# Optimization experiments

Hardware: AMD Instinct MI355X
Metric: run time of the kernel (lower is better)

Reference implementation:

```python
import jax, jax.numpy as jnp
import numpy as np

EMBED_DIM = 1024
NUM_HEADS = 16
HEAD_DIM = EMBED_DIM // NUM_HEADS


def setup_inputs() -> dict:
    key = jax.random.key(0)
    ks = jax.random.split(key, 9)
    B, S, D = 2, 2048, EMBED_DIM
    scale = 1.0 / np.sqrt(D)
    x = jax.random.normal(ks[0], (B, S, D), dtype=jnp.float32)
    # Linear params (torch nn.Linear: y = x @ W.T + b); store W as [out, in]
    Wq = jax.random.normal(ks[1], (D, D), dtype=jnp.float32) * scale
    bq = jnp.zeros((D,), dtype=jnp.float32)
    Wk = jax.random.normal(ks[2], (D, D), dtype=jnp.float32) * scale
    bk = jnp.zeros((D,), dtype=jnp.float32)
    Wv = jax.random.normal(ks[3], (D, D), dtype=jnp.float32) * scale
    bv = jnp.zeros((D,), dtype=jnp.float32)
    Wo = jax.random.normal(ks[4], (D, D), dtype=jnp.float32) * scale
    bo = jnp.zeros((D,), dtype=jnp.float32)
    return {"x": x, "Wq": Wq, "bq": bq, "Wk": Wk, "bk": bk,
            "Wv": Wv, "bv": bv, "Wo": Wo, "bo": bo}


def reference(x, Wq, bq, Wk, bk, Wv, bv, Wo, bo):
    B, S, D = x.shape
    H, Hd = NUM_HEADS, HEAD_DIM
    scaling = Hd ** -0.5
    # projections (torch Linear: x @ W.T + b)
    q = (x @ Wq.T + bq).reshape(B, S, H, Hd).transpose(0, 2, 1, 3)  # [B,H,S,Hd]
    k = (x @ Wk.T + bk).reshape(B, S, H, Hd).transpose(0, 2, 1, 3)
    v = (x @ Wv.T + bv).reshape(B, S, H, Hd).transpose(0, 2, 1, 3)
    # full score matrix, as in the original (no flash tiling)
    scores = jnp.einsum('bhqd,bhkd->bhqk', q, k) * scaling  # [B,H,S,S]
    attn = jax.nn.softmax(scores, axis=-1)
    # dropout is identity in eval mode
    out = jnp.einsum('bhqk,bhkd->bhqd', attn, v)  # [B,H,S,Hd]
    out = out.transpose(0, 2, 1, 3).reshape(B, S, D)
    return out @ Wo.T + bo
```

## Files before the change

kernel.cpp:

```cpp
#include <hip/hip_runtime.h>
#include <stdint.h>

typedef unsigned short u16;
typedef short short8 __attribute__((ext_vector_type(8)));
typedef float f32x4 __attribute__((ext_vector_type(4)));
typedef float f32x16 __attribute__((ext_vector_type(16)));
typedef float f32x2 __attribute__((ext_vector_type(2)));

__device__ __forceinline__ u16 f2bf_fast(float f) {
  union { float f; uint32_t u; } x;
  x.f = f;
  return (u16)((x.u + 0x8000u) >> 16);
}

__device__ __forceinline__ uint32_t pack2bf(float lo, float hi) {
  union { float f; uint32_t u; } a, b;
  a.f = lo; b.f = hi;
  return __builtin_amdgcn_perm(b.u + 0x8000u, a.u + 0x8000u, 0x07060302u);
}

__device__ __forceinline__ float bf2f(uint32_t u) {
  union { uint32_t u; float f; } x;
  x.u = u << 16;
  return x.f;
}

__device__ __forceinline__ uint32_t cvtpk(float lo, float hi) {
  uint32_t r;
  asm("v_cvt_pk_bf16_f32 %0, %1, %2" : "=v"(r) : "v"(lo), "v"(hi));
  return r;
}

__device__ __forceinline__ void permswap(uint32_t& a, uint32_t& b) {
  asm("v_permlane32_swap_b32 %0, %1" : "+v"(a), "+v"(b));
}

__device__ __forceinline__ void gload_lds16(const void* g, void* l) {
  __builtin_amdgcn_global_load_lds(
      (const __attribute__((address_space(1))) void*)g,
      (__attribute__((address_space(3))) void*)l, 16, 0, 0);
}

__device__ __forceinline__ f32x4 mfma16(short8 a, short8 b, f32x4 c) {
  return __builtin_amdgcn_mfma_f32_16x16x32_bf16(a, b, c, 0, 0, 0);
}

__device__ __forceinline__ f32x16 mfma32(short8 a, short8 b, f32x16 c) {
  return __builtin_amdgcn_mfma_f32_32x32x16_bf16(a, b, c, 0, 0, 0);
}

__device__ __forceinline__ short8 ldfrag(const u16* base, int tile, int kc,
                                         int lane) {
  return *(const short8*)(base + ((((tile << 5) + kc) << 6) + lane) * 8);
}

#define QSCALE 0.18033688011112042f

__global__ void pack_all(const float* __restrict__ x, const float* __restrict__ wq,
                         const float* __restrict__ wk, const float* __restrict__ wv,
                         const float* __restrict__ wo, u16* __restrict__ xp,
                         u16* __restrict__ wp) {
  const int gi = blockIdx.x * 256 + threadIdx.x;
  const int lane = gi & 63;
  const int kc = (gi >> 6) & 31;
  const int rt = gi >> 11;
  const int col = kc * 32 + (lane >> 4) * 8;
  const float* src;
  int row;
  if (rt < 256) {
    src = x;
    row = rt * 16 + (lane & 15);
  } else {
    const int wti = rt - 256;
    const int widx = wti >> 6;
    src = (widx == 0) ? wq : (widx == 1) ? wk : (widx == 2) ? wv : wo;
    row = (wti & 63) * 16 + (lane & 15);
  }
  const float4* p = (const float4*)(src + (size_t)row * 1024 + col);
  const float4 v0 = p[0], v1 = p[1];
  uint4 o;
  o.x = pack2bf(v0.x, v0.y);
  o.y = pack2bf(v0.z, v0.w);
  o.z = pack2bf(v1.x, v1.y);
  o.w = pack2bf(v1.z, v1.w);
  u16* dst = (rt < 256) ? xp : wp;
  const int og = (rt < 256) ? gi : gi - 524288;
  ((uint4*)dst)[og] = o;
}

__global__ __launch_bounds__(256, 3) void proj_qkv(
    const u16* __restrict__ xp, const u16* __restrict__ wp,
    const float* __restrict__ bq, const float* __restrict__ bk,
    const float* __restrict__ bv, u16* __restrict__ qw, u16* __restrict__ kw,
    u16* __restrict__ vw) {
  const int gid = blockIdx.x * 4 + (threadIdx.x >> 6);
  const int lane = threadIdx.x & 63;
  const int quad = lane >> 4, l15 = lane & 15;
  const bool isQK = gid < 2048;
  int at0, bt0, bm, bn;
  const u16 *Ap, *Bp;
  if (isQK) {
    bn = gid >> 6; bm = gid & 63;
    Ap = xp; at0 = bm * 4;
    Bp = wp; bt0 = bn * 4;
  } else {
    const int h = gid - 2048;
    bn = h & 63; bm = h >> 6;
    Ap = wp; at0 = 128 + bm * 4;
    Bp = xp; bt0 = bn * 4;
  }

  f32x4 acc[4][4] = {};
  short8 af[2][4], bf[2][4];
#pragma unroll
  for (int mt = 0; mt < 4; ++mt) af[0][mt] = ldfrag(Ap, at0 + mt, 0, lane);
#pragma unroll
  for (int nt = 0; nt < 4; ++nt) bf[0][nt] = ldfrag(Bp, bt0 + nt, 0, lane);

#pragma unroll 4
  for (int kc = 0; kc < 32; ++kc) {
    const int cur = kc & 1, nxt = cur ^ 1;
    if (kc < 31) {
#pragma unroll
      for (int mt = 0; mt < 4; ++mt)
        af[nxt][mt] = ldfrag(Ap, at0 + mt, kc + 1, lane);
#pragma unroll
      for (int nt = 0; nt < 4; ++nt)
        bf[nxt][nt] = ldfrag(Bp, bt0 + nt, kc + 1, lane);
    }
#pragma unroll
    for (int mt = 0; mt < 4; ++mt)
#pragma unroll
      for (int nt = 0; nt < 4; ++nt)
        acc[mt][nt] = mfma16(af[cur][mt], bf[cur][nt], acc[mt][nt]);
  }

#pragma unroll
  for (int nt = 0; nt < 4; ++nt) {
    const int n = bn * 64 + nt * 16 + l15;
#pragma unroll
    for (int mt = 0; mt < 4; ++mt)
#pragma unroll
      for (int r = 0; r < 4; ++r) {
        const int m = bm * 64 + mt * 16 + quad * 4 + r;
        const float a = acc[mt][nt][r];
        if (isQK) {
          const bool isQ = (bn < 16);
          const int nn = isQ ? n : n - 1024;
          const float v = isQ ? (a + bq[nn]) * QSCALE : a + bk[nn];
          u16* op = isQ ? qw : kw;
          const int b = m >> 11, s = m & 2047, hh = nn >> 6, d = nn & 63;
          op[((size_t)((b * 16 + hh) * 2048 + s)) * 64 + d] = f2bf_fast(v);
        } else {
          const float v = a + bv[m];
          const int b = n >> 11, s = n & 2047;
          vw[((size_t)(b * 1024 + m)) * 2048 + s] = f2bf_fast(v);
        }
      }
  }
}

__global__ __launch_bounds__(256, 4) void attn_kernel(
    const u16* __restrict__ Q, const u16* __restrict__ Kt,
    const u16* __restrict__ Vt, u16* __restrict__ op0, u16* __restrict__ op1,
    float* __restrict__ lp) {
  __shared__ __align__(16) u16 Sm[16384];
  const int tid = threadIdx.x, lane = tid & 63, w = tid >> 6;
  const int l31 = lane & 31, hi = lane >> 5, l7 = lane & 7;
  const int qt = blockIdx.x;
  const int bh = blockIdx.y >> 1;
  const int ks = blockIdx.y & 1;

  const char* Qb = (const char*)(Q + ((size_t)bh * 2048 + qt * 128) * 64);
  const char* Kb = (const char*)(Kt + ((size_t)bh * 2048 + ks * 1024) * 64);
  const char* Vb = (const char*)(Vt + (size_t)bh * 64 * 2048 + ks * 1024);

  auto stageKV = [&](int kt, int b) {
    u16* Kl = Sm + b * 4096;
    u16* Vl = Sm + 8192 + b * 4096;
#pragma unroll
    for (int i = 0; i < 2; ++i) {
      const int G = (w * 2 + i) * 64 + lane;
      const int r = G >> 3, sl = G & 7;
      gload_lds16(Kb + (size_t)(kt * 64 + r) * 128 + ((sl ^ (r & 7)) * 16),
                  &Kl[G * 8]);
      gload_lds16(Vb + (size_t)r * 4096 + kt * 128 + ((sl ^ (r & 7)) * 16),
                  &Vl[G * 8]);
    }
  };

#pragma unroll
  for (int i = 0; i < 4; ++i) {
    const int G = (w * 4 + i) * 64 + lane;
    const int row = G >> 3, sl = G & 7;
    u16* qdst = (G < 512) ? (Sm + 4096) : (Sm + 12288);
    gload_lds16(Qb + (size_t)row * 128 + ((sl ^ (row & 7)) * 16),
                &qdst[(G & 511) * 8]);
  }
  stageKV(0, 0);
  __syncthreads();

  const u16* qreg = (w < 2) ? (Sm + 4096) : (Sm + 12288);
  const int qr0 = (w & 1) * 32;
  short8 aq[4];
#pragma unroll
  for (int ds = 0; ds < 4; ++ds)
    aq[ds] = *(const short8*)&qreg[(qr0 + l31) * 64 + (((ds << 1) + hi) ^ l7) * 8];
  __syncthreads();

  f32x16 ot[2] = {};
  f32x2 l2 = {0.f, 0.f};

  for (int kt = 0; kt < 16; ++kt) {
    const int buf = kt & 1;
    if (kt < 15) stageKV(kt + 1, buf ^ 1);
    const u16* Kl = Sm + buf * 4096;
    const u16* Vl = Sm + 8192 + buf * 4096;

#pragma unroll
    for (int t = 0; t < 2; ++t) {
      f32x16 st = {};
#pragma unroll
      for (int ds = 0; ds < 4; ++ds) {
        short8 kf = *(const short8*)&Kl[(t * 32 + l31) * 64 +
                                        (((ds << 1) + hi) ^ l7) * 8];
        st = mfma32(kf, aq[ds], st);
      }
      float e[16];
#pragma unroll
      for (int i = 0; i < 16; ++i) e[i] = __builtin_amdgcn_exp2f(st[i]);
#pragma unroll
      for (int i = 0; i < 8; ++i) l2 += (f32x2){e[2 * i], e[2 * i + 1]};

      uint32_t p01 = cvtpk(e[0], e[1]),   p23 = cvtpk(e[2], e[3]);
      uint32_t p45 = cvtpk(e[4], e[5]),   p67 = cvtpk(e[6], e[7]);
      uint32_t p89 = cvtpk(e[8], e[9]),   pAB = cvtpk(e[10], e[11]);
      uint32_t pCD = cvtpk(e[12], e[13]), pEF = cvtpk(e[14], e[15]);
      permswap(p01, p45);
      permswap(p23, p67);
      permswap(p89, pCD);
      permswap(pAB, pEF);
      union { uint32_t u[4]; short8 s; } b0, b1;
      b0.u[0] = p01; b0.u[1] = p23; b0.u[2] = p45; b0.u[3] = p67;
      b1.u[0] = p89; b1.u[1] = pAB; b1.u[2] = pCD; b1.u[3] = pEF;

#pragma unroll
      for (int dt = 0; dt < 2; ++dt) {
#pragma unroll
        for (int s2 = 0; s2 < 2; ++s2) {
          short8 vf = *(const short8*)&Vl[(dt * 32 + l31) * 64 +
                                          ((((t * 2 + s2) << 1) + hi) ^ l7) * 8];
          ot[dt] = mfma32(vf, s2 ? b1.s : b0.s, ot[dt]);
        }
      }
    }
    if (kt < 15) __syncthreads();
  }

  const int b = bh >> 4, h = bh & 15;
  u16* op = ks ? op1 : op0;
  float l = l2.x + l2.y;
  l += __shfl_xor(l, 32);
  const int srow = qt * 128 + w * 32 + l31;
  if (hi == 0) lp[((size_t)(ks * 32 + bh)) * 2048 + srow] = l;
  const int rt = b * 128 + qt * 8 + w * 2 + (l31 >> 4);
#pragma unroll
  for (int dt = 0; dt < 2; ++dt) {
    const int kc = h * 2 + dt;
#pragma unroll
    for (int g = 0; g < 4; ++g) {
      const int ln = (lane & 15) + 16 * g;
      uint2 ov;
      ov.x = cvtpk(ot[dt][4 * g + 0], ot[dt][4 * g + 1]);
      ov.y = cvtpk(ot[dt][4 * g + 2], ot[dt][4 * g + 3]);
      *(uint2*)(op + ((size_t)((rt * 32 + kc) * 64 + ln)) * 8 + hi * 4) = ov;
    }
  }
}

__global__ void attn_combine(const u16* __restrict__ op0,
                             const u16* __restrict__ op1,
                             const float* __restrict__ lp,
                             u16* __restrict__ awp) {
  const int g = blockIdx.x * 256 + threadIdx.x;
  const int ln = g & 63;
  const int kc = (g >> 6) & 31;
  const int rt = g >> 11;
  const int row = rt * 16 + (ln & 15);
  const int b = row >> 11, s = row & 2047;
  const int h = kc >> 1;
  const int lidx = (b * 16 + h) * 2048 + s;
  const float inv = __builtin_amdgcn_rcpf(lp[lidx] + lp[lidx + 65536]);
  const uint4 a0 = ((const uint4*)op0)[g];
  const uint4 a1 = ((const uint4*)op1)[g];
  uint4 o;
  o.x = pack2bf((bf2f(a0.x) + bf2f(a1.x)) * inv,
                (bf2f(a0.x >> 16) + bf2f(a1.x >> 16)) * inv);
  o.y = pack2bf((bf2f(a0.y) + bf2f(a1.y)) * inv,
                (bf2f(a0.y >> 16) + bf2f(a1.y >> 16)) * inv);
  o.z = pack2bf((bf2f(a0.z) + bf2f(a1.z)) * inv,
                (bf2f(a0.z >> 16) + bf2f(a1.z >> 16)) * inv);
  o.w = pack2bf((bf2f(a0.w) + bf2f(a1.w)) * inv,
                (bf2f(a0.w >> 16) + bf2f(a1.w >> 16)) * inv);
  ((uint4*)awp)[g] = o;
}

__global__ __launch_bounds__(256, 3) void out_proj(const u16* __restrict__ awp,
                                                   const u16* __restrict__ wp,
                                                   const float* __restrict__ bo,
                                                   float* __restrict__ out) {
  const int gid = blockIdx.x * 4 + (threadIdx.x >> 6);
  const int lane = threadIdx.x & 63;
  const int quad = lane >> 4, l15 = lane & 15;
  const int bm = gid & 63, bnn = gid >> 6;
  const int at0 = bm * 4, bt0 = 192 + bnn * 2;

  f32x4 acc[4][2] = {};
  short8 af[2][4], bf[2][2];
#pragma unroll
  for (int mt = 0; mt < 4; ++mt) af[0][mt] = ldfrag(awp, at0 + mt, 0, lane);
#pragma unroll
  for (int nt = 0; nt < 2; ++nt) bf[0][nt] = ldfrag(wp, bt0 + nt, 0, lane);

#pragma unroll 4
  for (int kc = 0; kc < 32; ++kc) {
    const int cur = kc & 1, nxt = cur ^ 1;
    if (kc < 31) {
#pragma unroll
      for (int mt = 0; mt < 4; ++mt)
        af[nxt][mt] = ldfrag(awp, at0 + mt, kc + 1, lane);
#pragma unroll
      for (int nt = 0; nt < 2; ++nt)
        bf[nxt][nt] = ldfrag(wp, bt0 + nt, kc + 1, lane);
    }
#pragma unroll
    for (int mt = 0; mt < 4; ++mt)
#pragma unroll
      for (int nt = 0; nt < 2; ++nt)
        acc[mt][nt] = mfma16(af[cur][mt], bf[cur][nt], acc[mt][nt]);
  }

#pragma unroll
  for (int nt = 0; nt < 2; ++nt) {
    const int n = bnn * 32 + nt * 16 + l15;
    const float bb = bo[n];
#pragma unroll
    for (int mt = 0; mt < 4; ++mt)
#pragma unroll
      for (int r = 0; r < 4; ++r) {
        const int m = bm * 64 + mt * 16 + quad * 4 + r;
        out[(size_t)m * 1024 + n] = acc[mt][nt][r] + bb;
      }
  }
}

extern "C" void kernel_launch(void* const* d_in, const int* in_sizes, int n_in,
                              void* d_out, int out_size, void* d_ws, size_t ws_size,
                              hipStream_t stream) {
  const float* x  = (const float*)d_in[0];
  const float* Wq = (const float*)d_in[1];
  const float* bq = (const float*)d_in[2];
  const float* Wk = (const float*)d_in[3];
  const float* bk = (const float*)d_in[4];
  const float* Wv = (const float*)d_in[5];
  const float* bv = (const float*)d_in[6];
  const float* Wo = (const float*)d_in[7];
  const float* bo = (const float*)d_in[8];

  const size_t M4 = (size_t)4 * 1024 * 1024;
  u16* xp  = (u16*)d_ws;
  u16* wp  = xp + M4;
  u16* qw  = wp + M4;
  u16* kw  = qw + M4;
  u16* vw  = kw + M4;
  u16* op1 = vw + M4;
  u16* awp = op1 + M4;
  float* lp = (float*)(awp + M4);
  u16* op0 = xp;

  pack_all<<<4096, 256, 0, stream>>>(x, Wq, Wk, Wv, Wo, xp, wp);

  proj_qkv<<<768, 256, 0, stream>>>(xp, wp, bq, bk, bv, qw, kw, vw);

  attn_kernel<<<dim3(16, 64), 256, 0, stream>>>(qw, kw, vw, op0, op1, lp);

  attn_combine<<<2048, 256, 0, stream>>>(op0, op1, lp, awp);

  out_proj<<<512, 256, 0, stream>>>(awp, wp, bo, (float*)d_out);
}
```

Baseline: 199.1 us.

## Stage projection GEMM tiles through LDS shared across waves with XCD-aware block mapping

The QKV and output projection GEMMs move from per-wave direct global fragment loads to block-level 128x128 tiles staged in LDS via global_load_lds. Each wave then reads its fragments from shared memory, so A and B tiles are reused across waves and global traffic drops. Block indices are remapped so neighbouring tiles land on the same XCD for better L2 reuse. The staging is single-buffered with two barriers per k-step, which removes the previous register double-buffering and may expose load latency.

```diff
diff --git a/kernel.cpp b/kernel.cpp
--- a/kernel.cpp
+++ b/kernel.cpp
@@ -47,11 +47,6 @@
 
 __device__ __forceinline__ f32x16 mfma32(short8 a, short8 b, f32x16 c) {
   return __builtin_amdgcn_mfma_f32_32x32x16_bf16(a, b, c, 0, 0, 0);
-}
-
-__device__ __forceinline__ short8 ldfrag(const u16* base, int tile, int kc,
-                                         int lane) {
-  return *(const short8*)(base + ((((tile << 5) + kc) << 6) + lane) * 8);
 }
 
 #define QSCALE 0.18033688011112042f
@@ -93,46 +88,65 @@
     const float* __restrict__ bq, const float* __restrict__ bk,
     const float* __restrict__ bv, u16* __restrict__ qw, u16* __restrict__ kw,
     u16* __restrict__ vw) {
-  const int gid = blockIdx.x * 4 + (threadIdx.x >> 6);
-  const int lane = threadIdx.x & 63;
+  __shared__ __align__(16) u16 As[8192];
+  __shared__ __align__(16) u16 Bs[8192];
+  const int tid = threadIdx.x, lane = tid & 63, w = tid >> 6;
   const int quad = lane >> 4, l15 = lane & 15;
-  const bool isQK = gid < 2048;
-  int at0, bt0, bm, bn;
+
+  const int bid = blockIdx.x;
+  const int work = (bid & 7) * 96 + (bid >> 3);
+  const bool isQK = work < 512;
+  int at0, bt0, bm2, bn2;
   const u16 *Ap, *Bp;
   if (isQK) {
-    bn = gid >> 6; bm = gid & 63;
-    Ap = xp; at0 = bm * 4;
-    Bp = wp; bt0 = bn * 4;
+    bm2 = work >> 4; bn2 = work & 15;
+    Ap = xp; at0 = bm2 * 8;
+    Bp = wp; bt0 = bn2 * 8;
   } else {
-    const int h = gid - 2048;
-    bn = h & 63; bm = h >> 6;
-    Ap = wp; at0 = 128 + bm * 4;
-    Bp = xp; bt0 = bn * 4;
-  }
+    const int h = work - 512;
+    bm2 = h >> 5; bn2 = h & 31;
+    Ap = wp; at0 = 128 + bm2 * 8;
+    Bp = xp; bt0 = bn2 * 8;
+  }
+  const int wr = w >> 1, wc = w & 1;
+  const int bm = bm2 * 2 + wr, bn = bn2 * 2 + wc;
 
   f32x4 acc[4][4] = {};
-  short8 af[2][4], bf[2][4];
-#pragma unroll
-  for (int mt = 0; mt < 4; ++mt) af[0][mt] = ldfrag(Ap, at0 + mt, 0, lane);
-#pragma unroll
-  for (int nt = 0; nt < 4; ++nt) bf[0][nt] = ldfrag(Bp, bt0 + nt, 0, lane);
-
-#pragma unroll 4
-  for (int kc = 0; kc < 32; ++kc) {
-    const int cur = kc & 1, nxt = cur ^ 1;
-    if (kc < 31) {
+
+  for (int ks = 0; ks < 16; ++ks) {
+    const int kc0 = ks * 2;
+#pragma unroll
+    for (int i = 0; i < 8; ++i) {
+      const int g = w * 8 + i;
+      const int gg = g & 15, t = gg >> 1, c = gg & 1;
+      const u16* src = (g < 16)
+          ? (Ap + ((((at0 + t) << 5) + kc0 + c) * 64 + lane) * 8)
+          : (Bp + ((((bt0 + t) << 5) + kc0 + c) * 64 + lane) * 8);
+      u16* dst = ((g < 16) ? As : Bs) + (gg * 64 + lane) * 8;
+      gload_lds16(src, dst);
+    }
+    __syncthreads();
+
+    short8 af[4][2], bf[4][2];
+#pragma unroll
+    for (int mt = 0; mt < 4; ++mt)
+#pragma unroll
+      for (int c = 0; c < 2; ++c)
+        af[mt][c] = *(const short8*)&As[((((wr * 4 + mt) << 1) + c) * 64 + lane) * 8];
+#pragma unroll
+    for (int nt = 0; nt < 4; ++nt)
+#pragma unroll
+      for (int c = 0; c < 2; ++c)
+        bf[nt][c] = *(const short8*)&Bs[((((wc * 4 + nt) << 1) + c) * 64 + lane) * 8];
+
+#pragma unroll
+    for (int c = 0; c < 2; ++c)
 #pragma unroll
       for (int mt = 0; mt < 4; ++mt)
-        af[nxt][mt] = ldfrag(Ap, at0 + mt, kc + 1, lane);
-#pragma unroll
-      for (int nt = 0; nt < 4; ++nt)
-        bf[nxt][nt] = ldfrag(Bp, bt0 + nt, kc + 1, lane);
-    }
-#pragma unroll
-    for (int mt = 0; mt < 4; ++mt)
-#pragma unroll
-      for (int nt = 0; nt < 4; ++nt)
-        acc[mt][nt] = mfma16(af[cur][mt], bf[cur][nt], acc[mt][nt]);
+#pragma unroll
+        for (int nt = 0; nt < 4; ++nt)
+          acc[mt][nt] = mfma16(af[mt][c], bf[nt][c], acc[mt][nt]);
+    __syncthreads();
   }
 
 #pragma unroll
@@ -305,50 +319,68 @@
   ((uint4*)awp)[g] = o;
 }
 
-__global__ __launch_bounds__(256, 3) void out_proj(const u16* __restrict__ awp,
+__global__ __launch_bounds__(512, 2) void out_proj(const u16* __restrict__ awp,
                                                    const u16* __restrict__ wp,
                                                    const float* __restrict__ bo,
                                                    float* __restrict__ out) {
-  const int gid = blockIdx.x * 4 + (threadIdx.x >> 6);
-  const int lane = threadIdx.x & 63;
+  __shared__ __align__(16) u16 As[8192];
+  __shared__ __align__(16) u16 Bs[8192];
+  const int tid = threadIdx.x, lane = tid & 63, w = tid >> 6;
   const int quad = lane >> 4, l15 = lane & 15;
-  const int bm = gid & 63, bnn = gid >> 6;
-  const int at0 = bm * 4, bt0 = 192 + bnn * 2;
+
+  const int bid = blockIdx.x;
+  const int work = (bid & 7) * 32 + (bid >> 3);
+  const int bm2 = work >> 3, bn2 = work & 7;
+  const int at0 = bm2 * 8, bt0 = 192 + bn2 * 8;
+  const int wr = w >> 2, wc = w & 3;
 
   f32x4 acc[4][2] = {};
-  short8 af[2][4], bf[2][2];
-#pragma unroll
-  for (int mt = 0; mt < 4; ++mt) af[0][mt] = ldfrag(awp, at0 + mt, 0, lane);
-#pragma unroll
-  for (int nt = 0; nt < 2; ++nt) bf[0][nt] = ldfrag(wp, bt0 + nt, 0, lane);
-
-#pragma unroll 4
-  for (int kc = 0; kc < 32; ++kc) {
-    const int cur = kc & 1, nxt = cur ^ 1;
-    if (kc < 31) {
+
+  for (int ks = 0; ks < 16; ++ks) {
+    const int kc0 = ks * 2;
+#pragma unroll
+    for (int i = 0; i < 4; ++i) {
+      const int g = w * 4 + i;
+      const int gg = g & 15, t = gg >> 1, c = gg & 1;
+      const u16* src = (g < 16)
+          ? (awp + ((((at0 + t) << 5) + kc0 + c) * 64 + lane) * 8)
+          : (wp + ((((bt0 + t) << 5) + kc0 + c) * 64 + lane) * 8);
+      u16* dst = ((g < 16) ? As : Bs) + (gg * 64 + lane) * 8;
+      gload_lds16(src, dst);
+    }
+    __syncthreads();
+
+    short8 af[4][2], bf[2][2];
+#pragma unroll
+    for (int mt = 0; mt < 4; ++mt)
+#pragma unroll
+      for (int c = 0; c < 2; ++c)
+        af[mt][c] = *(const short8*)&As[((((wr * 4 + mt) << 1) + c) * 64 + lane) * 8];
+#pragma unroll
+    for (int nt = 0; nt < 2; ++nt)
+#pragma unroll
+      for (int c = 0; c < 2; ++c)
+        bf[nt][c] = *(const short8*)&Bs[((((wc * 2 + nt) << 1) + c) * 64 + lane) * 8];
+
+#pragma unroll
+    for (int c = 0; c < 2; ++c)
 #pragma unroll
       for (int mt = 0; mt < 4; ++mt)
-        af[nxt][mt] = ldfrag(awp, at0 + mt, kc + 1, lane);
-#pragma unroll
-      for (int nt = 0; nt < 2; ++nt)
-        bf[nxt][nt] = ldfrag(wp, bt0 + nt, kc + 1, lane);
-    }
+#pragma unroll
+        for (int nt = 0; nt < 2; ++nt)
+          acc[mt][nt] = mfma16(af[mt][c], bf[nt][c], acc[mt][nt]);
+    __syncthreads();
+  }
+
+#pragma unroll
+  for (int nt = 0; nt < 2; ++nt) {
+    const int n = bn2 * 128 + wc * 32 + nt * 16 + l15;
+    const float bb = bo[n];
 #pragma unroll
     for (int mt = 0; mt < 4; ++mt)
 #pragma unroll
-      for (int nt = 0; nt < 2; ++nt)
-        acc[mt][nt] = mfma16(af[cur][mt], bf[cur][nt], acc[mt][nt]);
-  }
-
-#pragma unroll
-  for (int nt = 0; nt < 2; ++nt) {
-    const int n = bnn * 32 + nt * 16 + l15;
-    const float bb = bo[n];
-#pragma unroll
-    for (int mt = 0; mt < 4; ++mt)
-#pragma unroll
       for (int r = 0; r < 4; ++r) {
-        const int m = bm * 64 + mt * 16 + quad * 4 + r;
+        const int m = bm2 * 128 + wr * 64 + mt * 16 + quad * 4 + r;
         out[(size_t)m * 1024 + n] = acc[mt][nt][r] + bb;
       }
   }
@@ -386,5 +418,5 @@
 
   attn_combine<<<2048, 256, 0, stream>>>(op0, op1, lp, awp);
 
-  out_proj<<<512, 256, 0, stream>>>(awp, wp, bo, (float*)d_out);
-}
+  out_proj<<<256, 512, 0, stream>>>(awp, wp, bo, (float*)d_out);
+}
```

Result: faster. 192.9 us (-3.1%).
